# Optimization experiments

Measured on AMD Instinct MI355X. Metric: run time of the kernel, lower is better.

Reference implementation:

```python
import jax, jax.numpy as jnp
import numpy as np

N_NODES = 50000
N_EDGES = 600000
D_IN = 128      # input_dim
D_EDGE = 128    # edge_dim
GAMMA, ZETA = -0.1, 1.1  # hard-concrete stretch params


def _spectral_norm(w):
    # torch spectral_norm divides weight by its top singular value
    s = np.linalg.svd(w, compute_uv=False)[0]
    return w / s


def setup_inputs() -> dict:
    key = jax.random.key(0)
    ks = jax.random.split(key, 8)
    node_feat = jax.random.normal(ks[0], (N_NODES, D_IN), dtype=jnp.float32)
    edge_index = jax.random.randint(ks[1], (2, N_EDGES), 0, N_NODES, dtype=jnp.int64)
    rng = np.random.default_rng(0)
    # kaiming-normal init then spectral normalization (applied once at setup)
    def kaiming(fan_in, shape):
        return (rng.standard_normal(shape) * np.sqrt(2.0 / fan_in)).astype(np.float32)
    W1 = jnp.asarray(_spectral_norm(kaiming(2 * D_IN + 1, (D_EDGE, 2 * D_IN + 1))))
    W2 = jnp.asarray(_spectral_norm(kaiming(D_EDGE, (D_EDGE, D_EDGE))))
    W3 = jnp.asarray(_spectral_norm(kaiming(D_EDGE, (1, D_EDGE))))
    b1 = jnp.zeros((D_EDGE,), jnp.float32)
    b2 = jnp.zeros((D_EDGE,), jnp.float32)
    b3 = jnp.zeros((1,), jnp.float32)
    return {"node_feat": node_feat, "edge_index": edge_index,
            "W1": W1, "b1": b1, "W2": W2, "b2": b2, "W3": W3, "b3": b3}


def reference(node_feat, edge_index, W1, b1, W2, b2, W3, b3):
    # L2-normalize node features
    nf = node_feat / (jnp.linalg.norm(node_feat, axis=-1, keepdims=True) + 1e-8)
    src, tgt = edge_index[0], edge_index[1]
    hs = nf[src]                      # [E, D_IN] gather
    ht = nf[tgt]                      # [E, D_IN] gather
    dist = jnp.linalg.norm(hs - ht, axis=-1)  # [E]
    edge_features = jnp.concatenate([hs, ht, dist[:, None]], axis=-1)  # [E, 2D+1]
    h = jax.nn.relu(edge_features @ W1.T + b1)
    h = jax.nn.relu(h @ W2.T + b2)
    logAlpha = (h @ W3.T + b3).squeeze(-1)    # [E]
    # hard-concrete deterministic (l0_test) gate
    edge_weights = jnp.clip(jax.nn.sigmoid(logAlpha) * (ZETA - GAMMA) + GAMMA, 0.0, 1.0)
    return edge_weights, logAlpha
```

## Files before the change

kernel.cpp:

```cpp
#include <hip/hip_runtime.h>


#define E_TOT 600000
#define NN    50000
#define DIN   128

typedef short bf16x8 __attribute__((ext_vector_type(8)));
typedef float f32x4  __attribute__((ext_vector_type(4)));

union FragU { uint4 q; unsigned int u[4]; bf16x8 v; };

__device__ __forceinline__ unsigned int f2bf(float x) {
  unsigned int b = __float_as_uint(x);
  return ((b + 0x7fffu + ((b >> 16) & 1u)) >> 16) & 0xffffu;
}

__device__ __forceinline__ void async_cp16(const uint4* g, uint4* l) {
  __builtin_amdgcn_global_load_lds((const __attribute__((address_space(1))) void*)g,
                                   (__attribute__((address_space(3))) void*)l, 16, 0, 0);
}

__global__ __launch_bounds__(256) void k_pre(const float* __restrict__ nf,
                                             const float* __restrict__ W1,
                                             const float* __restrict__ W2,
                                             unsigned short* __restrict__ nfb,
                                             unsigned int* __restrict__ B1,
                                             unsigned int* __restrict__ B2) {
  if (blockIdx.x < 6250) {
    const int wv = threadIdx.x >> 6, l = threadIdx.x & 63;
    const int h = l >> 5, r = l & 31;
    const int node = blockIdx.x * 8 + wv * 2 + h;
    const float4* row = (const float4*)(nf + (size_t)node * DIN);
    float4 v = row[r];
    float ss = v.x * v.x + v.y * v.y + v.z * v.z + v.w * v.w;
    #pragma unroll
    for (int msk = 1; msk < 32; msk <<= 1) ss += __shfl_xor(ss, msk);
    const float inv = 1.0f / (sqrtf(ss) + 1e-8f);
    uint2 o;
    o.x = f2bf(v.x * inv) | (f2bf(v.y * inv) << 16);
    o.y = f2bf(v.z * inv) | (f2bf(v.w * inv) << 16);
    ((uint2*)(nfb + (size_t)node * DIN))[r] = o;
  } else {
    const int id = (blockIdx.x - 6250) * 256 + threadIdx.x;
    if (id < 16384) {
      const int dw = id & 3, lane = (id >> 2) & 63, nt = (id >> 8) & 7, s = id >> 11;
      const int n = nt * 16 + (lane & 15);
      const int k0 = (lane >> 4) * 8 + s * 32 + dw * 2;
      B1[id] = f2bf(W1[n * 257 + k0]) | (f2bf(W1[n * 257 + k0 + 1]) << 16);
    } else {
      const int i2 = id - 16384;
      const int dw = i2 & 3, lane = (i2 >> 2) & 63, nt = (i2 >> 8) & 7, s = i2 >> 11;
      const int n = nt * 16 + (lane & 15);
      const int k0 = (lane >> 4) * 8 + s * 32 + dw * 2;
      B2[i2] = f2bf(W2[n * 128 + k0]) | (f2bf(W2[n * 128 + k0 + 1]) << 16);
    }
  }
}

__global__ __launch_bounds__(256, 3) void k_main(
    const unsigned short* __restrict__ nfb, const int* __restrict__ ei,
    const unsigned int* __restrict__ B1, const unsigned int* __restrict__ B2,
    const float* __restrict__ W1, const float* __restrict__ b1,
    const float* __restrict__ b2, const float* __restrict__ W3,
    const float* __restrict__ b3, float* __restrict__ out) {
  __shared__ unsigned int lds[4096 + 4 * 2048];
  const int tid = threadIdx.x;
  const int wv = tid >> 6, l = tid & 63, m = l & 15, a = l >> 4;
  char* sH0 = (char*)(lds + 4096) + wv * 8192;
  char* sH1 = sH0 + 4096;

  const int w0 = ei[l];
  const bool is64 = __all((l & 1) == 0 || w0 == 0);

  const int e0 = blockIdx.x * 128 + wv * 32 + m;
  const int ec0 = min(e0, E_TOT - 1);
  const int ec1 = min(e0 + 16, E_TOT - 1);
  int ns0, nt0_, ns1, nt1_;
  if (is64) { ns0 = ei[2 * ec0]; nt0_ = ei[2 * (E_TOT + ec0)];
              ns1 = ei[2 * ec1]; nt1_ = ei[2 * (E_TOT + ec1)]; }
  else      { ns0 = ei[ec0];     nt0_ = ei[E_TOT + ec0];
              ns1 = ei[ec1];     nt1_ = ei[E_TOT + ec1]; }
  ns0 = min(max(ns0, 0), NN - 1);  nt0_ = min(max(nt0_, 0), NN - 1);
  ns1 = min(max(ns1, 0), NN - 1);  nt1_ = min(max(nt1_, 0), NN - 1);

  const uint4* rs0 = (const uint4*)(nfb + (size_t)ns0 * DIN);
  const uint4* rt0 = (const uint4*)(nfb + (size_t)nt0_ * DIN);
  const uint4* rs1 = (const uint4*)(nfb + (size_t)ns1 * DIN);
  const uint4* rt1 = (const uint4*)(nfb + (size_t)nt1_ * DIN);
  uint4 hsv0[4], htv0[4], hsv1[4], htv1[4];
  #pragma unroll
  for (int s = 0; s < 4; ++s) {
    hsv0[s] = rs0[a + 4 * s]; htv0[s] = rt0[a + 4 * s];
    hsv1[s] = rs1[a + 4 * s]; htv1[s] = rt1[a + 4 * s];
  }

  float dist_r0[4], dist_r1[4];
  {
    float dp0 = 0.f, dp1 = 0.f;
    #pragma unroll
    for (int i = 0; i < 4; ++i) {
      const unsigned int* h0u = (const unsigned int*)&hsv0[i];
      const unsigned int* t0u = (const unsigned int*)&htv0[i];
      const unsigned int* h1u = (const unsigned int*)&hsv1[i];
      const unsigned int* t1u = (const unsigned int*)&htv1[i];
      #pragma unroll
      for (int j = 0; j < 4; ++j) {
        float dlo = __uint_as_float(h0u[j] << 16) - __uint_as_float(t0u[j] << 16);
        float dhi = __uint_as_float(h0u[j] & 0xffff0000u) - __uint_as_float(t0u[j] & 0xffff0000u);
        dp0 = fmaf(dlo, dlo, dp0); dp0 = fmaf(dhi, dhi, dp0);
        float elo = __uint_as_float(h1u[j] << 16) - __uint_as_float(t1u[j] << 16);
        float ehi = __uint_as_float(h1u[j] & 0xffff0000u) - __uint_as_float(t1u[j] & 0xffff0000u);
        dp1 = fmaf(elo, elo, dp1); dp1 = fmaf(ehi, ehi, dp1);
      }
    }
    dp0 += __shfl_xor(dp0, 16); dp0 += __shfl_xor(dp0, 32);
    dp1 += __shfl_xor(dp1, 16); dp1 += __shfl_xor(dp1, 32);
    const float d0 = sqrtf(dp0), d1 = sqrtf(dp1);
    #pragma unroll
    for (int r = 0; r < 4; ++r) {
      dist_r0[r] = __shfl(d0, a * 4 + r);
      dist_r1[r] = __shfl(d1, a * 4 + r);
    }
  }

  f32x4 acc0[8], acc1[8];
  #pragma unroll
  for (int nt = 0; nt < 8; ++nt) {
    acc0[nt] = (f32x4){0.f, 0.f, 0.f, 0.f};
    acc1[nt] = (f32x4){0.f, 0.f, 0.f, 0.f};
  }

  const uint4* g1 = (const uint4*)B1;
  const uint4* g2 = (const uint4*)B2;
  uint4* sB0 = (uint4*)lds;
  uint4* sB1b = sB0 + 512;

  #define STAGE(c) do {                                                      \
    const uint4* gs_ = ((c) < 8) ? (g1 + (c) * 512) : (g2 + ((c) - 8) * 512);\
    uint4* db_ = (((c) & 1) ? sB1b : sB0);                                   \
    async_cp16(gs_ + wv * 64 + l, db_ + wv * 64);                            \
    async_cp16(gs_ + 256 + wv * 64 + l, db_ + 256 + wv * 64);                \
  } while (0)

  STAGE(0);
  __syncthreads();

  #pragma unroll
  for (int st = 0; st < 12; ++st) {
    if (st < 11) STAGE(st + 1);

    FragU af0, af1;
    if (st < 4)      { af0.q = hsv0[st];     af1.q = hsv1[st]; }
    else if (st < 8) { af0.q = htv0[st - 4]; af1.q = htv1[st - 4]; }
    else {
      const int s2 = st - 8;
      const int col = (16 * a + 64 * s2) ^ ((m & 7) << 4);
      af0.q = *(const uint4*)(sH0 + m * 256 + col);
      af1.q = *(const uint4*)(sH1 + m * 256 + col);
    }

    const uint4* sB = (st & 1) ? sB1b : sB0;
    #pragma unroll
    for (int nt = 0; nt < 8; ++nt) {
      FragU bfr; bfr.q = sB[nt * 64 + l];
      acc0[nt] = __builtin_amdgcn_mfma_f32_16x16x32_bf16(af0.v, bfr.v, acc0[nt], 0, 0, 0);
      acc1[nt] = __builtin_amdgcn_mfma_f32_16x16x32_bf16(af1.v, bfr.v, acc1[nt], 0, 0, 0);
    }

    if (st == 7) {
      #pragma unroll
      for (int nt = 0; nt < 8; ++nt) {
        const int n = nt * 16 + m;
        const float b1v = b1[n];
        const float w1l = W1[n * 257 + 256];
        #pragma unroll
        for (int r = 0; r < 4; ++r) {
          const int row = 4 * a + r;
          const int cb = (2 * n) ^ ((row & 7) << 4);
          float v0 = fmaxf(acc0[nt][r] + b1v + w1l * dist_r0[r], 0.f);
          float v1 = fmaxf(acc1[nt][r] + b1v + w1l * dist_r1[r], 0.f);
          *(unsigned short*)(sH0 + row * 256 + cb) = (unsigned short)f2bf(v0);
          *(unsigned short*)(sH1 + row * 256 + cb) = (unsigned short)f2bf(v1);
        }
        acc0[nt] = (f32x4){0.f, 0.f, 0.f, 0.f};
        acc1[nt] = (f32x4){0.f, 0.f, 0.f, 0.f};
      }
    }
    __syncthreads();
  }

  float p0[4] = {0.f, 0.f, 0.f, 0.f}, p1[4] = {0.f, 0.f, 0.f, 0.f};
  #pragma unroll
  for (int nt = 0; nt < 8; ++nt) {
    const int n = nt * 16 + m;
    const float b2v = b2[n];
    const float w3v = W3[n];
    #pragma unroll
    for (int r = 0; r < 4; ++r) {
      p0[r] = fmaf(fmaxf(acc0[nt][r] + b2v, 0.f), w3v, p0[r]);
      p1[r] = fmaf(fmaxf(acc1[nt][r] + b2v, 0.f), w3v, p1[r]);
    }
  }
  #pragma unroll
  for (int r = 0; r < 4; ++r) {
    #pragma unroll
    for (int msk = 1; msk < 16; msk <<= 1) {
      p0[r] += __shfl_xor(p0[r], msk);
      p1[r] += __shfl_xor(p1[r], msk);
    }
  }
  if (m == 0) {
    const float b3v = b3[0];
    #pragma unroll
    for (int t = 0; t < 2; ++t) {
      #pragma unroll
      for (int r = 0; r < 4; ++r) {
        const int eo = blockIdx.x * 128 + wv * 32 + t * 16 + a * 4 + r;
        if (eo < E_TOT) {
          const float la = (t ? p1[r] : p0[r]) + b3v;
          const float sg = 1.f / (1.f + __expf(-la));
          out[eo] = fminf(fmaxf(sg * 1.2f - 0.1f, 0.f), 1.f);
          out[E_TOT + eo] = la;
        }
      }
    }
  }
}

extern "C" void kernel_launch(void* const* d_in, const int* in_sizes, int n_in,
                              void* d_out, int out_size, void* d_ws, size_t ws_size,
                              hipStream_t stream) {
  const float* node_feat = (const float*)d_in[0];
  const int*   edge_idx  = (const int*)d_in[1];
  const float* W1 = (const float*)d_in[2];
  const float* b1 = (const float*)d_in[3];
  const float* W2 = (const float*)d_in[4];
  const float* b2 = (const float*)d_in[5];
  const float* W3 = (const float*)d_in[6];
  const float* b3 = (const float*)d_in[7];
  float* out = (float*)d_out;

  unsigned char* ws = (unsigned char*)d_ws;
  unsigned short* nfb = (unsigned short*)(ws);
  unsigned int*   B1  = (unsigned int*)(ws + 12800000);
  unsigned int*   B2  = (unsigned int*)(ws + 12800000 + 65536);

  hipLaunchKernelGGL(k_pre, dim3(6346), dim3(256), 0, stream,
                     node_feat, W1, W2, nfb, B1, B2);
  hipLaunchKernelGGL(k_main, dim3(4688), dim3(256), 0, stream,
                     nfb, edge_idx, B1, B2, W1, b1, b2, W3, b3, out);
}
```

Baseline: 191.6 us.

## Compute edge distance via MFMA dot product and fold dist/bias into GEMM

Replaces the scalar per-lane squared-difference loop with MFMA dot products hs·ht, deriving distance as sqrt(2-2·dot) since rows are unit-normalized. The distance weight and bias b1 are folded into an extra 9th K-stage of the first GEMM (dist and a constant 1.0 as extra A-columns), so the epilogue no longer loads W1/b1 or applies the affine term. This adds one MFMA stage and relies on the unit-norm identity, which loses precision for nearly identical nodes and rounds the bias and distance to bf16.

```diff
diff --git a/kernel.cpp b/kernel.cpp
--- a/kernel.cpp
+++ b/kernel.cpp
@@ -22,6 +22,7 @@
 
 __global__ __launch_bounds__(256) void k_pre(const float* __restrict__ nf,
                                              const float* __restrict__ W1,
+                                             const float* __restrict__ b1,
                                              const float* __restrict__ W2,
                                              unsigned short* __restrict__ nfb,
                                              unsigned int* __restrict__ B1,
@@ -42,13 +43,19 @@
     ((uint2*)(nfb + (size_t)node * DIN))[r] = o;
   } else {
     const int id = (blockIdx.x - 6250) * 256 + threadIdx.x;
-    if (id < 16384) {
+    if (id < 18432) {
       const int dw = id & 3, lane = (id >> 2) & 63, nt = (id >> 8) & 7, s = id >> 11;
       const int n = nt * 16 + (lane & 15);
-      const int k0 = (lane >> 4) * 8 + s * 32 + dw * 2;
-      B1[id] = f2bf(W1[n * 257 + k0]) | (f2bf(W1[n * 257 + k0 + 1]) << 16);
+      if (s < 8) {
+        const int k0 = (lane >> 4) * 8 + s * 32 + dw * 2;
+        B1[id] = f2bf(W1[n * 257 + k0]) | (f2bf(W1[n * 257 + k0 + 1]) << 16);
+      } else {
+        B1[id] = ((lane >> 4) == 0 && dw == 0)
+                   ? (f2bf(W1[n * 257 + 256]) | (f2bf(b1[n]) << 16))
+                   : 0u;
+      }
     } else {
-      const int i2 = id - 16384;
+      const int i2 = id - 18432;
       const int dw = i2 & 3, lane = (i2 >> 2) & 63, nt = (i2 >> 8) & 7, s = i2 >> 11;
       const int n = nt * 16 + (lane & 15);
       const int k0 = (lane >> 4) * 8 + s * 32 + dw * 2;
@@ -60,7 +67,6 @@
 __global__ __launch_bounds__(256, 3) void k_main(
     const unsigned short* __restrict__ nfb, const int* __restrict__ ei,
     const unsigned int* __restrict__ B1, const unsigned int* __restrict__ B2,
-    const float* __restrict__ W1, const float* __restrict__ b1,
     const float* __restrict__ b2, const float* __restrict__ W3,
     const float* __restrict__ b3, float* __restrict__ out) {
   __shared__ unsigned int lds[4096 + 4 * 2048];
@@ -94,33 +100,31 @@
     hsv1[s] = rs1[a + 4 * s]; htv1[s] = rt1[a + 4 * s];
   }
 
-  float dist_r0[4], dist_r1[4];
+  unsigned int dfw0, dfw1;
   {
-    float dp0 = 0.f, dp1 = 0.f;
-    #pragma unroll
-    for (int i = 0; i < 4; ++i) {
-      const unsigned int* h0u = (const unsigned int*)&hsv0[i];
-      const unsigned int* t0u = (const unsigned int*)&htv0[i];
-      const unsigned int* h1u = (const unsigned int*)&hsv1[i];
-      const unsigned int* t1u = (const unsigned int*)&htv1[i];
-      #pragma unroll
-      for (int j = 0; j < 4; ++j) {
-        float dlo = __uint_as_float(h0u[j] << 16) - __uint_as_float(t0u[j] << 16);
-        float dhi = __uint_as_float(h0u[j] & 0xffff0000u) - __uint_as_float(t0u[j] & 0xffff0000u);
-        dp0 = fmaf(dlo, dlo, dp0); dp0 = fmaf(dhi, dhi, dp0);
-        float elo = __uint_as_float(h1u[j] << 16) - __uint_as_float(t1u[j] << 16);
-        float ehi = __uint_as_float(h1u[j] & 0xffff0000u) - __uint_as_float(t1u[j] & 0xffff0000u);
-        dp1 = fmaf(elo, elo, dp1); dp1 = fmaf(ehi, ehi, dp1);
-      }
-    }
-    dp0 += __shfl_xor(dp0, 16); dp0 += __shfl_xor(dp0, 32);
-    dp1 += __shfl_xor(dp1, 16); dp1 += __shfl_xor(dp1, 32);
-    const float d0 = sqrtf(dp0), d1 = sqrtf(dp1);
+    f32x4 ad0 = (f32x4){0.f, 0.f, 0.f, 0.f}, ad1 = (f32x4){0.f, 0.f, 0.f, 0.f};
+    #pragma unroll
+    for (int s = 0; s < 4; ++s) {
+      FragU a0, b0, a1, b1f;
+      a0.q = hsv0[s]; b0.q = htv0[s]; a1.q = hsv1[s]; b1f.q = htv1[s];
+      ad0 = __builtin_amdgcn_mfma_f32_16x16x32_bf16(a0.v, b0.v, ad0, 0, 0, 0);
+      ad1 = __builtin_amdgcn_mfma_f32_16x16x32_bf16(a1.v, b1f.v, ad1, 0, 0, 0);
+    }
+    const int srcl = 16 * (m >> 2) + m;
+    float ds0[4], ds1[4];
     #pragma unroll
     for (int r = 0; r < 4; ++r) {
-      dist_r0[r] = __shfl(d0, a * 4 + r);
-      dist_r1[r] = __shfl(d1, a * 4 + r);
-    }
+      ds0[r] = __shfl(ad0[r], srcl);
+      ds1[r] = __shfl(ad1[r], srcl);
+    }
+    const float sel0 = (m & 2) ? ((m & 1) ? ds0[3] : ds0[2])
+                               : ((m & 1) ? ds0[1] : ds0[0]);
+    const float sel1 = (m & 2) ? ((m & 1) ? ds1[3] : ds1[2])
+                               : ((m & 1) ? ds1[1] : ds1[0]);
+    const float dist0 = sqrtf(fmaxf(2.f - 2.f * sel0, 0.f));
+    const float dist1 = sqrtf(fmaxf(2.f - 2.f * sel1, 0.f));
+    dfw0 = (a == 0) ? (f2bf(dist0) | 0x3F800000u) : 0u;
+    dfw1 = (a == 0) ? (f2bf(dist1) | 0x3F800000u) : 0u;
   }
 
   f32x4 acc0[8], acc1[8];
@@ -136,7 +140,7 @@
   uint4* sB1b = sB0 + 512;
 
   #define STAGE(c) do {                                                      \
-    const uint4* gs_ = ((c) < 8) ? (g1 + (c) * 512) : (g2 + ((c) - 8) * 512);\
+    const uint4* gs_ = ((c) < 9) ? (g1 + (c) * 512) : (g2 + ((c) - 9) * 512);\
     uint4* db_ = (((c) & 1) ? sB1b : sB0);                                   \
     async_cp16(gs_ + wv * 64 + l, db_ + wv * 64);                            \
     async_cp16(gs_ + 256 + wv * 64 + l, db_ + 256 + wv * 64);                \
@@ -146,14 +150,17 @@
   __syncthreads();
 
   #pragma unroll
-  for (int st = 0; st < 12; ++st) {
-    if (st < 11) STAGE(st + 1);
+  for (int st = 0; st < 13; ++st) {
+    if (st < 12) STAGE(st + 1);
 
     FragU af0, af1;
     if (st < 4)      { af0.q = hsv0[st];     af1.q = hsv1[st]; }
     else if (st < 8) { af0.q = htv0[st - 4]; af1.q = htv1[st - 4]; }
-    else {
-      const int s2 = st - 8;
+    else if (st == 8) {
+      af0.u[0] = dfw0; af0.u[1] = 0; af0.u[2] = 0; af0.u[3] = 0;
+      af1.u[0] = dfw1; af1.u[1] = 0; af1.u[2] = 0; af1.u[3] = 0;
+    } else {
+      const int s2 = st - 9;
       const int col = (16 * a + 64 * s2) ^ ((m & 7) << 4);
       af0.q = *(const uint4*)(sH0 + m * 256 + col);
       af1.q = *(const uint4*)(sH1 + m * 256 + col);
@@ -167,18 +174,16 @@
       acc1[nt] = __builtin_amdgcn_mfma_f32_16x16x32_bf16(af1.v, bfr.v, acc1[nt], 0, 0, 0);
     }
 
-    if (st == 7) {
+    if (st == 8) {
       #pragma unroll
       for (int nt = 0; nt < 8; ++nt) {
         const int n = nt * 16 + m;
-        const float b1v = b1[n];
-        const float w1l = W1[n * 257 + 256];
         #pragma unroll
         for (int r = 0; r < 4; ++r) {
           const int row = 4 * a + r;
           const int cb = (2 * n) ^ ((row & 7) << 4);
-          float v0 = fmaxf(acc0[nt][r] + b1v + w1l * dist_r0[r], 0.f);
-          float v1 = fmaxf(acc1[nt][r] + b1v + w1l * dist_r1[r], 0.f);
+          const float v0 = fmaxf(acc0[nt][r], 0.f);
+          const float v1 = fmaxf(acc1[nt][r], 0.f);
           *(unsigned short*)(sH0 + row * 256 + cb) = (unsigned short)f2bf(v0);
           *(unsigned short*)(sH1 + row * 256 + cb) = (unsigned short)f2bf(v1);
         }
@@ -243,10 +248,10 @@
   unsigned char* ws = (unsigned char*)d_ws;
   unsigned short* nfb = (unsigned short*)(ws);
   unsigned int*   B1  = (unsigned int*)(ws + 12800000);
-  unsigned int*   B2  = (unsigned int*)(ws + 12800000 + 65536);
-
-  hipLaunchKernelGGL(k_pre, dim3(6346), dim3(256), 0, stream,
-                     node_feat, W1, W2, nfb, B1, B2);
+  unsigned int*   B2  = (unsigned int*)(ws + 12800000 + 73728);
+
+  hipLaunchKernelGGL(k_pre, dim3(6354), dim3(256), 0, stream,
+                     node_feat, W1, b1, W2, nfb, B1, B2);
   hipLaunchKernelGGL(k_main, dim3(4688), dim3(256), 0, stream,
-                     nfb, edge_idx, B1, B2, W1, b1, b2, W3, b3, out);
-}
+                     nfb, edge_idx, B1, B2, b2, W3, b3, out);
+}
```

Result: faster. 185.4 us (-3.2%).
